# Kernel optimization log

Hardware: AMD Instinct MI355X
Metric: run time of the kernel (lower is better)

Reference implementation:

```python
import jax, jax.numpy as jnp
import numpy as np

B, S, K, N, GROUPS, GS = 4, 2048, 4096, 4096, 32, 128


def setup_inputs() -> dict:
    key = jax.random.key(0)
    k1, k2, k3, k4, k5 = jax.random.split(key, 5)
    x = jax.random.normal(k1, (B, S, K), dtype=jnp.float32)
    # int8-stored quantized weights in [-128, 127], layout [K, N] (in_features, out_features)
    weight_int8 = jax.random.randint(k2, (K, N), -128, 128, dtype=jnp.int32)
    # per-group, per-output-column positive scales
    scales = (jax.random.uniform(k3, (GROUPS, N), dtype=jnp.float32) * 0.01 + 1e-4)
    bias = jax.random.normal(k4, (N,), dtype=jnp.float32) * 0.02
    # column reordering permutation (high-sensitivity cols first in the real module)
    col_indices = jax.random.permutation(k5, K).astype(jnp.int32)
    return {"x": x, "scales": scales, "bias": bias,
            "weight_int8": weight_int8, "col_indices": col_indices,
            "group_size": GS}


def reference(x, scales, bias, weight_int8, col_indices, group_size):
    orig_shape = x.shape
    k = x.shape[-1]
    x2 = x.reshape(-1, k)                      # [M, K]
    # CPR column reordering of the activations (weights are stored pre-reordered)
    x_reordered = x2[:, col_indices]           # [M, K]
    # per-group dequant: scale row-group g applies to rows [g*gs, (g+1)*gs) of W
    s_full = jnp.repeat(scales, group_size, axis=0)[:k]          # [K, N]
    w_deq = weight_int8.astype(x.dtype) * s_full                 # [K, N]
    y = x_reordered @ w_deq + bias                               # [M, N]
    return y.reshape(*orig_shape[:-1], y.shape[-1])
```

## Files before the change

kernel.cpp:

```cpp
#include <hip/hip_runtime.h>
#include <hip/hip_bf16.h>

#define M_DIM 8192
#define N_DIM 4096
#define K_DIM 4096
#define NT (K_DIM / 32)

typedef __bf16 bf16x8 __attribute__((ext_vector_type(8)));
typedef float f32x4 __attribute__((ext_vector_type(4)));
typedef unsigned short ushort8v __attribute__((ext_vector_type(8)));

typedef const __attribute__((address_space(1))) void gv_t;
typedef __attribute__((address_space(3))) void lv_t;

static __device__ __forceinline__ unsigned short f2bf(float f) {
  unsigned u = __builtin_bit_cast(unsigned, f);
  u += 0x7fffu + ((u >> 16) & 1u);
  return (unsigned short)(u >> 16);
}

__global__ void k_pinv(const int* __restrict__ ci, int* __restrict__ pinv) {
  int k = blockIdx.x * 256 + threadIdx.x;
  if (k < K_DIM) pinv[ci[k]] = k;
}

__global__ void k_cvt(const float* __restrict__ x, unsigned short* __restrict__ xb) {
  const long n4 = (long)M_DIM * K_DIM / 4;
  for (long i = (long)blockIdx.x * 256 + threadIdx.x; i < n4; i += 2048L * 256) {
    float4 v = *(const float4*)(x + i * 4);
    ushort4 o;
    o.x = f2bf(v.x); o.y = f2bf(v.y); o.z = f2bf(v.z); o.w = f2bf(v.w);
    *(ushort4*)(xb + i * 4) = o;
  }
}

__global__ void k_w2t(const int* __restrict__ w, const float* __restrict__ scales,
                      const int* __restrict__ pinv, unsigned short* __restrict__ w2t) {
  __shared__ int tile[64 * 68];
  __shared__ int grp[64];
  __shared__ int krow[64];
  const int n0 = blockIdx.x * 64;
  const int c0 = blockIdx.y * 64;
  const int t = threadIdx.x;
  if (t < 64) {
    int kk = pinv[c0 + t];
    krow[t] = kk;
    grp[t] = kk >> 7;
  }
  __syncthreads();
  {
    const int ci = t >> 2, q = t & 3;
    const int kk = krow[ci];
    const int* src = w + (long)kk * N_DIM + n0 + q * 16;
#pragma unroll
    for (int j = 0; j < 4; ++j) {
      int4 v = *(const int4*)(src + j * 4);
      *(int4*)&tile[ci * 68 + q * 16 + j * 4] = v;
    }
  }
  __syncthreads();
  {
    const int nj = t >> 2, cq = t & 3;
    const int n = n0 + nj;
    unsigned short outv[16];
#pragma unroll
    for (int i = 0; i < 16; ++i) {
      int cii = cq * 16 + i;
      float f = (float)tile[cii * 68 + nj] * scales[grp[cii] * N_DIM + n];
      outv[i] = f2bf(f);
    }
    unsigned short* dst = w2t + (long)n * K_DIM + c0 + cq * 16;
    *(ushort8v*)(dst)     = *(ushort8v*)&outv[0];
    *(ushort8v*)(dst + 8) = *(ushort8v*)&outv[8];
  }
}

__global__ __launch_bounds__(512, 2) void k_gemm(const unsigned short* __restrict__ A,
                                                 const unsigned short* __restrict__ Bt,
                                                 const float* __restrict__ bias,
                                                 float* __restrict__ C) {
  __shared__ __attribute__((aligned(16))) char lds[3 * 32768];

  const int bid = blockIdx.x;
  const int swz = (bid & 7) * 64 + (bid >> 3);
  const int by = swz >> 4;
  const int bx = swz & 15;

  const int tid = threadIdx.x;
  const int l = tid & 63;
  const int w = tid >> 6;
  const int wr = w >> 2;
  const int wc = w & 3;
  const int r4 = l & 15;
  const int kb = (l >> 4) << 4;
  const int rmask = (r4 & 14) << 3;

  const int wmask = ((tid >> 3) & 7) << 4;
  const char* srcA[2];
  const char* srcB[2];
  {
    const char* Ab = (const char*)A + (size_t)(by * 256) * (K_DIM * 2);
    const char* Bb = (const char*)Bt + (size_t)(bx * 256) * (K_DIM * 2);
#pragma unroll
    for (int j = 0; j < 2; ++j) {
      int L = j * 8192 + tid * 16;
      int lg = L ^ wmask;
      int row = lg >> 6, kbo = lg & 63;
      srcA[j] = Ab + (size_t)row * (K_DIM * 2) + kbo;
      srcB[j] = Bb + (size_t)row * (K_DIM * 2) + kbo;
    }
  }
  const int stgoff = tid * 16;

  const int aoff = (((wr * 128 + r4) << 6) + kb) ^ rmask;
  const int boff = (((wc * 64  + r4) << 6) + kb) ^ rmask;

  f32x4 acc[8][4];
  const f32x4 z = {0.f, 0.f, 0.f, 0.f};
#pragma unroll
  for (int mi = 0; mi < 8; ++mi)
#pragma unroll
    for (int ni = 0; ni < 4; ++ni) acc[mi][ni] = z;

#pragma unroll
  for (int tt = 0; tt < 2; ++tt) {
    char* ab = lds + tt * 32768;
    char* bb = ab + 16384;
#pragma unroll
    for (int j = 0; j < 2; ++j)
      __builtin_amdgcn_global_load_lds((gv_t*)(srcA[j] + tt * 64), (lv_t*)(ab + j * 8192 + stgoff), 16, 0, 0);
#pragma unroll
    for (int j = 0; j < 2; ++j)
      __builtin_amdgcn_global_load_lds((gv_t*)(srcB[j] + tt * 64), (lv_t*)(bb + j * 8192 + stgoff), 16, 0, 0);
  }
  asm volatile("s_waitcnt vmcnt(4)" ::: "memory");
  __builtin_amdgcn_sched_barrier(0);
  __builtin_amdgcn_s_barrier();
  __builtin_amdgcn_sched_barrier(0);

  bf16x8 fA[4], fB[4], gA1[4];
#pragma unroll
  for (int mi = 0; mi < 4; ++mi) fA[mi] = *(const bf16x8*)(lds + aoff + mi * 1024);
#pragma unroll
  for (int ni = 0; ni < 4; ++ni) fB[ni] = *(const bf16x8*)(lds + 16384 + boff + ni * 1024);

  int cur = 0;
  for (int t = 0; t < NT; ++t) {
    char* ab = lds + cur * 32768;
    char* bb = ab + 16384;
    int stg = cur + 2; if (stg >= 3) stg -= 3;
    char* sab = lds + stg * 32768;
    char* sbb = sab + 16384;
    int nxt = cur + 1; if (nxt >= 3) nxt -= 3;
    char* nab = lds + nxt * 32768;
    char* nbb = nab + 16384;
    const long koff = (long)(t + 2) * 64;

    if (t + 2 < NT) {
      __builtin_amdgcn_global_load_lds((gv_t*)(srcA[0] + koff), (lv_t*)(sab + stgoff), 16, 0, 0);
      __builtin_amdgcn_global_load_lds((gv_t*)(srcA[1] + koff), (lv_t*)(sab + 8192 + stgoff), 16, 0, 0);
    }
#pragma unroll
    for (int mi = 0; mi < 4; ++mi)
      gA1[mi] = *(const bf16x8*)(ab + aoff + 4096 + mi * 1024);

    __builtin_amdgcn_s_setprio(1);
#pragma unroll
    for (int mi = 0; mi < 4; ++mi)
#pragma unroll
      for (int ni = 0; ni < 4; ++ni)
        acc[mi][ni] = __builtin_amdgcn_mfma_f32_16x16x32_bf16(fA[mi], fB[ni], acc[mi][ni], 0, 0, 0);
    __builtin_amdgcn_s_setprio(0);

    if (t < NT - 2)       asm volatile("s_waitcnt vmcnt(2)" ::: "memory");
    else if (t == NT - 2) asm volatile("s_waitcnt vmcnt(0)" ::: "memory");
    __builtin_amdgcn_sched_barrier(0);
    __builtin_amdgcn_s_barrier();
    __builtin_amdgcn_sched_barrier(0);

    if (t + 2 < NT) {
      __builtin_amdgcn_global_load_lds((gv_t*)(srcB[0] + koff), (lv_t*)(sbb + stgoff), 16, 0, 0);
      __builtin_amdgcn_global_load_lds((gv_t*)(srcB[1] + koff), (lv_t*)(sbb + 8192 + stgoff), 16, 0, 0);
    }
    if (t + 1 < NT) {
#pragma unroll
      for (int mi = 0; mi < 4; ++mi)
        fA[mi] = *(const bf16x8*)(nab + aoff + mi * 1024);
    }

    __builtin_amdgcn_s_setprio(1);
#pragma unroll
    for (int mi = 0; mi < 4; ++mi)
#pragma unroll
      for (int ni = 0; ni < 4; ++ni)
        acc[4 + mi][ni] = __builtin_amdgcn_mfma_f32_16x16x32_bf16(gA1[mi], fB[ni], acc[4 + mi][ni], 0, 0, 0);
    __builtin_amdgcn_s_setprio(0);

    if (t + 1 < NT) {
#pragma unroll
      for (int ni = 0; ni < 4; ++ni)
        fB[ni] = *(const bf16x8*)(nbb + boff + ni * 1024);
    }
    __builtin_amdgcn_sched_barrier(0);
    __builtin_amdgcn_s_barrier();
    __builtin_amdgcn_sched_barrier(0);

    cur = nxt;
  }

  const int row0 = by * 256 + wr * 128 + ((l >> 4) << 2);
  const int col0 = bx * 256 + wc * 64 + r4;
#pragma unroll
  for (int ni = 0; ni < 4; ++ni) {
    const int col = col0 + ni * 16;
    const float bv = bias[col];
#pragma unroll
    for (int mi = 0; mi < 8; ++mi) {
#pragma unroll
      for (int r = 0; r < 4; ++r)
        C[(size_t)(row0 + mi * 16 + r) * N_DIM + col] = acc[mi][ni][r] + bv;
    }
  }
}

__global__ void k_fallback(const float* __restrict__ x, const float* __restrict__ scales,
                           const float* __restrict__ bias, const int* __restrict__ w,
                           const int* __restrict__ ci, float* __restrict__ out) {
  const int n = blockIdx.x * 256 + threadIdx.x;
  const int m0 = blockIdx.y * 32;
  float acc[32];
#pragma unroll
  for (int i = 0; i < 32; ++i) acc[i] = 0.f;
  for (int k = 0; k < K_DIM; ++k) {
    int c = ci[k];
    float wv = (float)w[(long)k * N_DIM + n] * scales[(k >> 7) * N_DIM + n];
#pragma unroll 8
    for (int mm = 0; mm < 32; ++mm)
      acc[mm] += x[(long)(m0 + mm) * K_DIM + c] * wv;
  }
  float bv = bias[n];
  for (int mm = 0; mm < 32; ++mm)
    out[(long)(m0 + mm) * N_DIM + n] = acc[mm] + bv;
}

extern "C" void kernel_launch(void* const* d_in, const int* in_sizes, int n_in,
                              void* d_out, int out_size, void* d_ws, size_t ws_size,
                              hipStream_t stream) {
  const float* x      = (const float*)d_in[0];
  const float* scales = (const float*)d_in[1];
  const float* bias   = (const float*)d_in[2];
  const int*   wq     = (const int*)d_in[3];
  const int*   ci     = (const int*)d_in[4];
  float* out = (float*)d_out;

  const size_t xb_bytes  = (size_t)M_DIM * K_DIM * 2;
  const size_t w2t_bytes = (size_t)N_DIM * K_DIM * 2;
  const size_t need = xb_bytes + w2t_bytes + (size_t)K_DIM * 4;

  if (ws_size < need) {
    k_fallback<<<dim3(N_DIM / 256, M_DIM / 32), 256, 0, stream>>>(x, scales, bias, wq, ci, out);
    return;
  }

  unsigned short* xb  = (unsigned short*)d_ws;
  unsigned short* w2t = (unsigned short*)((char*)d_ws + xb_bytes);
  int* pinv           = (int*)((char*)d_ws + xb_bytes + w2t_bytes);

  k_pinv<<<K_DIM / 256, 256, 0, stream>>>(ci, pinv);
  k_cvt<<<2048, 256, 0, stream>>>(x, xb);
  k_w2t<<<dim3(N_DIM / 64, K_DIM / 64), 256, 0, stream>>>(wq, scales, pinv, w2t);
  k_gemm<<<(M_DIM / 256) * (N_DIM / 256), 512, 0, stream>>>(xb, w2t, bias, out);
}
```

Measured before the change: 313.4 us.

## Switch GEMM to BK=64 double-buffered LDS pipeline with new swizzle

Restructures the bf16 MFMA GEMM main loop from a triple-buffered K=32 pipeline to a double-buffered K=64 one with 64KB per stage. Each iteration does four MFMA sub-phases with interleaved LDS fragment loads, halving the iteration count and the number of barriers per unit of K. The LDS swizzle is changed to match 128-byte rows. The trade-off is 128KB of LDS, which may reduce occupancy below the two blocks per CU that launch_bounds requests. It also relies on a full vmcnt(0) wait each iteration, with loads for the next tile issued only one iteration ahead.

```diff
diff --git a/kernel.cpp b/kernel.cpp
--- a/kernel.cpp
+++ b/kernel.cpp
@@ -4,7 +4,7 @@
 #define M_DIM 8192
 #define N_DIM 4096
 #define K_DIM 4096
-#define NT (K_DIM / 32)
+#define NT (K_DIM / 64)
 
 typedef __bf16 bf16x8 __attribute__((ext_vector_type(8)));
 typedef float f32x4 __attribute__((ext_vector_type(4)));
@@ -79,7 +79,7 @@
                                                  const unsigned short* __restrict__ Bt,
                                                  const float* __restrict__ bias,
                                                  float* __restrict__ C) {
-  __shared__ __attribute__((aligned(16))) char lds[3 * 32768];
+  __shared__ __attribute__((aligned(16))) char lds[2 * 65536];
 
   const int bid = blockIdx.x;
   const int swz = (bid & 7) * 64 + (bid >> 3);
@@ -93,27 +93,17 @@
   const int wc = w & 3;
   const int r4 = l & 15;
   const int kb = (l >> 4) << 4;
-  const int rmask = (r4 & 14) << 3;
 
   const int wmask = ((tid >> 3) & 7) << 4;
-  const char* srcA[2];
-  const char* srcB[2];
-  {
-    const char* Ab = (const char*)A + (size_t)(by * 256) * (K_DIM * 2);
-    const char* Bb = (const char*)Bt + (size_t)(bx * 256) * (K_DIM * 2);
-#pragma unroll
-    for (int j = 0; j < 2; ++j) {
-      int L = j * 8192 + tid * 16;
-      int lg = L ^ wmask;
-      int row = lg >> 6, kbo = lg & 63;
-      srcA[j] = Ab + (size_t)row * (K_DIM * 2) + kbo;
-      srcB[j] = Bb + (size_t)row * (K_DIM * 2) + kbo;
-    }
-  }
+  const int kbo = ((tid & 7) * 16) ^ wmask;
+  const char* srcA = (const char*)A + (size_t)(by * 256 + (tid >> 3)) * (K_DIM * 2) + kbo;
+  const char* srcB = (const char*)Bt + (size_t)(bx * 256 + (tid >> 3)) * (K_DIM * 2) + kbo;
   const int stgoff = tid * 16;
 
-  const int aoff = (((wr * 128 + r4) << 6) + kb) ^ rmask;
-  const int boff = (((wc * 64  + r4) << 6) + kb) ^ rmask;
+  const int R0A = wr * 128 + r4;
+  const int R0B = wc * 64 + r4;
+  const int aoff0 = ((R0A << 7) + kb) ^ ((R0A & 7) << 4);
+  const int boff0 = ((R0B << 7) + kb) ^ ((R0B & 7) << 4);
 
   f32x4 acc[8][4];
   const f32x4 z = {0.f, 0.f, 0.f, 0.f};
@@ -123,89 +113,103 @@
     for (int ni = 0; ni < 4; ++ni) acc[mi][ni] = z;
 
 #pragma unroll
-  for (int tt = 0; tt < 2; ++tt) {
-    char* ab = lds + tt * 32768;
-    char* bb = ab + 16384;
-#pragma unroll
-    for (int j = 0; j < 2; ++j)
-      __builtin_amdgcn_global_load_lds((gv_t*)(srcA[j] + tt * 64), (lv_t*)(ab + j * 8192 + stgoff), 16, 0, 0);
-#pragma unroll
-    for (int j = 0; j < 2; ++j)
-      __builtin_amdgcn_global_load_lds((gv_t*)(srcB[j] + tt * 64), (lv_t*)(bb + j * 8192 + stgoff), 16, 0, 0);
-  }
-  asm volatile("s_waitcnt vmcnt(4)" ::: "memory");
+  for (int j = 0; j < 4; ++j)
+    __builtin_amdgcn_global_load_lds((gv_t*)(srcA + j * 524288), (lv_t*)(lds + j * 8192 + stgoff), 16, 0, 0);
+#pragma unroll
+  for (int j = 0; j < 4; ++j)
+    __builtin_amdgcn_global_load_lds((gv_t*)(srcB + j * 524288), (lv_t*)(lds + 32768 + j * 8192 + stgoff), 16, 0, 0);
+#pragma unroll
+  for (int j = 0; j < 4; ++j)
+    __builtin_amdgcn_global_load_lds((gv_t*)(srcA + 128 + j * 524288), (lv_t*)(lds + 65536 + j * 8192 + stgoff), 16, 0, 0);
+#pragma unroll
+  for (int j = 0; j < 4; ++j)
+    __builtin_amdgcn_global_load_lds((gv_t*)(srcB + 128 + j * 524288), (lv_t*)(lds + 65536 + 32768 + j * 8192 + stgoff), 16, 0, 0);
+
+  asm volatile("s_waitcnt vmcnt(8)" ::: "memory");
   __builtin_amdgcn_sched_barrier(0);
   __builtin_amdgcn_s_barrier();
   __builtin_amdgcn_sched_barrier(0);
 
-  bf16x8 fA[4], fB[4], gA1[4];
-#pragma unroll
-  for (int mi = 0; mi < 4; ++mi) fA[mi] = *(const bf16x8*)(lds + aoff + mi * 1024);
-#pragma unroll
-  for (int ni = 0; ni < 4; ++ni) fB[ni] = *(const bf16x8*)(lds + 16384 + boff + ni * 1024);
-
-  int cur = 0;
+  bf16x8 aR[2][4], bR[2][4];
+#pragma unroll
+  for (int mi = 0; mi < 4; ++mi) aR[0][mi] = *(const bf16x8*)(lds + aoff0 + mi * 2048);
+#pragma unroll
+  for (int ni = 0; ni < 4; ++ni) bR[0][ni] = *(const bf16x8*)(lds + 32768 + boff0 + ni * 2048);
+
   for (int t = 0; t < NT; ++t) {
-    char* ab = lds + cur * 32768;
-    char* bb = ab + 16384;
-    int stg = cur + 2; if (stg >= 3) stg -= 3;
-    char* sab = lds + stg * 32768;
-    char* sbb = sab + 16384;
-    int nxt = cur + 1; if (nxt >= 3) nxt -= 3;
-    char* nab = lds + nxt * 32768;
-    char* nbb = nab + 16384;
-    const long koff = (long)(t + 2) * 64;
-
-    if (t + 2 < NT) {
-      __builtin_amdgcn_global_load_lds((gv_t*)(srcA[0] + koff), (lv_t*)(sab + stgoff), 16, 0, 0);
-      __builtin_amdgcn_global_load_lds((gv_t*)(srcA[1] + koff), (lv_t*)(sab + 8192 + stgoff), 16, 0, 0);
-    }
-#pragma unroll
-    for (int mi = 0; mi < 4; ++mi)
-      gA1[mi] = *(const bf16x8*)(ab + aoff + 4096 + mi * 1024);
-
-    __builtin_amdgcn_s_setprio(1);
-#pragma unroll
-    for (int mi = 0; mi < 4; ++mi)
-#pragma unroll
-      for (int ni = 0; ni < 4; ++ni)
-        acc[mi][ni] = __builtin_amdgcn_mfma_f32_16x16x32_bf16(fA[mi], fB[ni], acc[mi][ni], 0, 0, 0);
-    __builtin_amdgcn_s_setprio(0);
-
-    if (t < NT - 2)       asm volatile("s_waitcnt vmcnt(2)" ::: "memory");
-    else if (t == NT - 2) asm volatile("s_waitcnt vmcnt(0)" ::: "memory");
+    const int cur = t & 1;
+    char* Ac = lds + cur * 65536;
+    char* Bc = Ac + 32768;
+    char* An = lds + (cur ^ 1) * 65536;
+    char* Bn = An + 32768;
+
+    if (t >= 1 && t + 1 < NT) {
+      const long ko = (long)(t + 1) * 128;
+#pragma unroll
+      for (int j = 0; j < 4; ++j)
+        __builtin_amdgcn_global_load_lds((gv_t*)(srcA + ko + j * 524288), (lv_t*)(An + j * 8192 + stgoff), 16, 0, 0);
+#pragma unroll
+      for (int j = 0; j < 4; ++j)
+        __builtin_amdgcn_global_load_lds((gv_t*)(srcB + ko + j * 524288), (lv_t*)(Bn + j * 8192 + stgoff), 16, 0, 0);
+    }
+#pragma unroll
+    for (int mi = 0; mi < 4; ++mi)
+      aR[1][mi] = *(const bf16x8*)(Ac + (aoff0 + 8192) + mi * 2048);
+    __builtin_amdgcn_s_setprio(1);
+#pragma unroll
+    for (int mi = 0; mi < 4; ++mi)
+#pragma unroll
+      for (int ni = 0; ni < 4; ++ni)
+        acc[mi][ni] = __builtin_amdgcn_mfma_f32_16x16x32_bf16(aR[0][mi], bR[0][ni], acc[mi][ni], 0, 0, 0);
+    __builtin_amdgcn_s_setprio(0);
+
+#pragma unroll
+    for (int mi = 0; mi < 4; ++mi)
+      aR[0][mi] = *(const bf16x8*)(Ac + (aoff0 ^ 64) + mi * 2048);
+#pragma unroll
+    for (int ni = 0; ni < 4; ++ni)
+      bR[1][ni] = *(const bf16x8*)(Bc + (boff0 ^ 64) + ni * 2048);
+    __builtin_amdgcn_s_setprio(1);
+#pragma unroll
+    for (int mi = 0; mi < 4; ++mi)
+#pragma unroll
+      for (int ni = 0; ni < 4; ++ni)
+        acc[4 + mi][ni] = __builtin_amdgcn_mfma_f32_16x16x32_bf16(aR[1][mi], bR[0][ni], acc[4 + mi][ni], 0, 0, 0);
+    __builtin_amdgcn_s_setprio(0);
+
+#pragma unroll
+    for (int mi = 0; mi < 4; ++mi)
+      aR[1][mi] = *(const bf16x8*)(Ac + ((aoff0 + 8192) ^ 64) + mi * 2048);
+    __builtin_amdgcn_s_setprio(1);
+#pragma unroll
+    for (int mi = 0; mi < 4; ++mi)
+#pragma unroll
+      for (int ni = 0; ni < 4; ++ni)
+        acc[mi][ni] = __builtin_amdgcn_mfma_f32_16x16x32_bf16(aR[0][mi], bR[1][ni], acc[mi][ni], 0, 0, 0);
+    __builtin_amdgcn_s_setprio(0);
+    asm volatile("s_waitcnt vmcnt(0)" ::: "memory");
     __builtin_amdgcn_sched_barrier(0);
     __builtin_amdgcn_s_barrier();
     __builtin_amdgcn_sched_barrier(0);
 
-    if (t + 2 < NT) {
-      __builtin_amdgcn_global_load_lds((gv_t*)(srcB[0] + koff), (lv_t*)(sbb + stgoff), 16, 0, 0);
-      __builtin_amdgcn_global_load_lds((gv_t*)(srcB[1] + koff), (lv_t*)(sbb + 8192 + stgoff), 16, 0, 0);
-    }
     if (t + 1 < NT) {
 #pragma unroll
       for (int mi = 0; mi < 4; ++mi)
-        fA[mi] = *(const bf16x8*)(nab + aoff + mi * 1024);
-    }
-
-    __builtin_amdgcn_s_setprio(1);
-#pragma unroll
-    for (int mi = 0; mi < 4; ++mi)
-#pragma unroll
-      for (int ni = 0; ni < 4; ++ni)
-        acc[4 + mi][ni] = __builtin_amdgcn_mfma_f32_16x16x32_bf16(gA1[mi], fB[ni], acc[4 + mi][ni], 0, 0, 0);
-    __builtin_amdgcn_s_setprio(0);
-
-    if (t + 1 < NT) {
-#pragma unroll
-      for (int ni = 0; ni < 4; ++ni)
-        fB[ni] = *(const bf16x8*)(nbb + boff + ni * 1024);
-    }
+        aR[0][mi] = *(const bf16x8*)(An + aoff0 + mi * 2048);
+#pragma unroll
+      for (int ni = 0; ni < 4; ++ni)
+        bR[0][ni] = *(const bf16x8*)(Bn + boff0 + ni * 2048);
+    }
+    __builtin_amdgcn_s_setprio(1);
+#pragma unroll
+    for (int mi = 0; mi < 4; ++mi)
+#pragma unroll
+      for (int ni = 0; ni < 4; ++ni)
+        acc[4 + mi][ni] = __builtin_amdgcn_mfma_f32_16x16x32_bf16(aR[1][mi], bR[1][ni], acc[4 + mi][ni], 0, 0, 0);
+    __builtin_amdgcn_s_setprio(0);
     __builtin_amdgcn_sched_barrier(0);
     __builtin_amdgcn_s_barrier();
     __builtin_amdgcn_sched_barrier(0);
-
-    cur = nxt;
   }
 
   const int row0 = by * 256 + wr * 128 + ((l >> 4) << 2);
```

After: 313.5 us. About the same (+0.0%).
